# Performance work log

Measured on AMD Instinct MI355X. Metric: run time of the kernel, lower is better.

## Reference

```python
import jax, jax.numpy as jnp
import numpy as np

N, E, F, H, O = 50000, 800000, 256, 128, 64


def setup_inputs() -> dict:
    key = jax.random.key(0)
    ks = jax.random.split(key, 8)
    x = jax.random.normal(ks[0], (N, F), jnp.float32)
    edge_index = jax.random.randint(ks[1], (2, E), 0, N, jnp.int32)
    batch = jnp.zeros((N,), jnp.int32)  # single graph
    s = 0.05
    W0 = jax.random.normal(ks[2], (F, H), jnp.float32) * s
    W1 = jax.random.normal(ks[3], (H, H), jnp.float32) * s
    W2 = jax.random.normal(ks[4], (H, H), jnp.float32) * s
    Wlin = jax.random.normal(ks[5], (H, O), jnp.float32) * s
    b0 = jnp.zeros((H,), jnp.float32)
    b1 = jnp.zeros((H,), jnp.float32)
    b2 = jnp.zeros((H,), jnp.float32)
    blin = jnp.zeros((O,), jnp.float32)
    return {"x": x, "edge_index": edge_index, "batch": batch,
            "W0": W0, "b0": b0, "W1": W1, "b1": b1, "W2": W2, "b2": b2,
            "Wlin": Wlin, "blin": blin}


def _gcn_norm(edge_index, n, dtype):
    # GCNConv: add self-loops, symmetric normalization D^-1/2 (A+I) D^-1/2
    loop = jnp.arange(n, dtype=edge_index.dtype)
    src = jnp.concatenate([edge_index[0], loop])
    dst = jnp.concatenate([edge_index[1], loop])
    deg = jax.ops.segment_sum(jnp.ones_like(dst, dtype=dtype), dst, num_segments=n)
    dinv = jnp.where(deg > 0, jax.lax.rsqrt(deg), 0.0)
    norm = dinv[src] * dinv[dst]  # [E+N]
    return src, dst, norm


def _gcn_conv(h, src, dst, norm, b, n):
    # gather-transform-scatter: message = norm * h[src], aggregate at dst
    msg = h[src] * norm[:, None]
    return jax.ops.segment_sum(msg, dst, num_segments=n) + b


def reference(x, edge_index, batch, W0, b0, W1, b1, W2, b2, Wlin, blin):
    n = x.shape[0]
    src, dst, norm = _gcn_norm(edge_index, n, x.dtype)
    h = _gcn_conv(x @ W0, src, dst, norm, b0, n)   # no inter-layer activation in source
    h = _gcn_conv(h @ W1, src, dst, norm, b1, n)
    h = _gcn_conv(h @ W2, src, dst, norm, b2, n)
    # dropout p=0.2 is identity in eval mode
    h = h @ Wlin + blin
    out = jax.ops.segment_max(h, batch, num_segments=1)  # global_max_pool, single graph
    return out
```

## Files before the change

### kernel.cpp

```cpp
#include <hip/hip_runtime.h>
#include <math.h>


typedef __attribute__((ext_vector_type(8))) _Float16 f16x8;
typedef __attribute__((ext_vector_type(4))) _Float16 f16x4;
typedef __attribute__((ext_vector_type(4))) float f32x4;

__device__ __forceinline__ unsigned enc_f32(float f) {
    unsigned u = __float_as_uint(f);
    return (u & 0x80000000u) ? ~u : (u | 0x80000000u);
}
__device__ __forceinline__ float dec_f32(unsigned e) {
    return (e & 0x80000000u) ? __uint_as_float(e & 0x7fffffffu)
                             : __uint_as_float(~e);
}
#define ENC_NEG_INF 0x007FFFFFu

__device__ __forceinline__ void mm2v_dev(const float* __restrict__ A,
                                         const float* __restrict__ B,
                                         int ldb, int bcol0,
                                         float* __restrict__ C,
                                         int ldc, int ccol0,
                                         _Float16* __restrict__ Wp, int pack,
                                         int vb, int tid,
                                         float* __restrict__ Bs,
                                         float* __restrict__ As) {
    const int r0 = vb * 4;
#pragma unroll
    for (int it = 0; it < 8; ++it) {
        int f = tid + it * 256;
        int row = f >> 4, c4 = (f & 15) * 4;
        *(float4*)&Bs[row * 64 + c4] = *(const float4*)&B[(size_t)row * ldb + bcol0 + c4];
    }
    if (tid < 128)
        *(float4*)&As[tid * 4] = *(const float4*)&A[(size_t)r0 * 128 + tid * 4];
    __syncthreads();
    const int n = tid & 63;
    const int rh = tid >> 6;
    float a0 = 0.f, a1 = 0.f, a2 = 0.f, a3 = 0.f;
#pragma unroll
    for (int k = 0; k < 128; k += 4) {
        a0 = fmaf(As[rh * 128 + k + 0], Bs[(k + 0) * 64 + n], a0);
        a1 = fmaf(As[rh * 128 + k + 1], Bs[(k + 1) * 64 + n], a1);
        a2 = fmaf(As[rh * 128 + k + 2], Bs[(k + 2) * 64 + n], a2);
        a3 = fmaf(As[rh * 128 + k + 3], Bs[(k + 3) * 64 + n], a3);
    }
    float acc = (a0 + a1) + (a2 + a3);
    const int kk = r0 + rh;
    if (pack) {
        int j = kk & 7;
        int l = ((kk >> 3) & 3) * 16 + (n & 15);
        int q = kk >> 5;
        int c = n >> 4;
        Wp[((size_t)(c * 8 + q) * 64 + l) * 8 + j] = (_Float16)acc;
    } else {
        C[(size_t)kk * ldc + ccol0 + n] = acc;
    }
}

__global__ __launch_bounds__(256) void kA(const float* __restrict__ W0,
                                          const float* __restrict__ W1,
                                          const float* __restrict__ W2,
                                          const float* __restrict__ Wl,
                                          const int* __restrict__ dst,
                                          int* __restrict__ T,
                                          float* __restrict__ W01,
                                          float* __restrict__ Q,
                                          int E, int NB, int chunk) {
    __shared__ float Bs[128 * 64];
    __shared__ float As[4 * 128];
    __shared__ int hist[512];
    const int b = blockIdx.x;
    const int tid = threadIdx.x;
    if (b < 64) {
        mm2v_dev(W0, W1, 128, 0, W01, 128, 0, nullptr, 0, b, tid, Bs, As);
    } else if (b < 128) {
        mm2v_dev(W0, W1, 128, 64, W01, 128, 64, nullptr, 0, b - 64, tid, Bs, As);
    } else if (b < 160) {
        mm2v_dev(W2, Wl, 64, 0, Q, 64, 0, nullptr, 0, b - 128, tid, Bs, As);
    } else {
        const int blk = b - 160;
        for (int i = tid; i < 512; i += 256) hist[i] = 0;
        __syncthreads();
        const int lo = blk * chunk, hi = min(E, lo + chunk);
        for (int e = lo + tid; e < hi; e += 256)
            atomicAdd(&hist[dst[e] >> 7], 1);
        __syncthreads();
        for (int bk = tid; bk < NB; bk += 256)
            T[bk * 256 + blk] = hist[bk];
    }
}

__global__ __launch_bounds__(1024) void k_scan1(const int* __restrict__ in,
                                                int* __restrict__ excl,
                                                int* __restrict__ bsums, int L) {
    __shared__ int sh[1024];
    int t = threadIdx.x;
    int i = blockIdx.x * 1024 + t;
    int v = (i < L) ? in[i] : 0;
    sh[t] = v;
    __syncthreads();
    for (int off = 1; off < 1024; off <<= 1) {
        int tv = (t >= off) ? sh[t - off] : 0;
        __syncthreads();
        sh[t] += tv;
        __syncthreads();
    }
    if (i < L) excl[i] = sh[t] - v;
    if (t == 1023) bsums[blockIdx.x] = sh[1023];
}

__global__ __launch_bounds__(1024) void k_scan23(int* __restrict__ excl,
                                                 const int* __restrict__ bsums,
                                                 int L) {
    __shared__ int sh[1024];
    const int t = threadIdx.x;
    sh[t] = (t < (int)blockIdx.x) ? bsums[t] : 0;
    __syncthreads();
    for (int off = 512; off > 0; off >>= 1) {
        if (t < off) sh[t] += sh[t + off];
        __syncthreads();
    }
    const int ofs = sh[0];
    int i = blockIdx.x * 1024 + t;
    if (i < L) excl[i] += ofs;
}

#define PBT 4096
__global__ __launch_bounds__(256) void kP(const int* __restrict__ src,
                                          const int* __restrict__ dst,
                                          const int* __restrict__ T2,
                                          unsigned* __restrict__ eb,
                                          int E, int NB, int chunk,
                                          const float* __restrict__ W01,
                                          const float* __restrict__ Q,
                                          const float* __restrict__ W1,
                                          const float* __restrict__ b0,
                                          const float* __restrict__ b1,
                                          const float* __restrict__ b2,
                                          const float* __restrict__ blin,
                                          const float* __restrict__ Wl,
                                          _Float16* __restrict__ wp,
                                          float* __restrict__ cv) {
    __shared__ int hist[512], lexc[512], pos[512], wpos[512];
    __shared__ unsigned sorted[PBT];
    __shared__ float Bs[128 * 64];
    __shared__ float As[4 * 128];
    __shared__ float t0s[128];
    __shared__ int nzf;
    const int t = threadIdx.x;
    const int b = blockIdx.x;
    if (b < 256) {
        const int blk = b;
        const int lo = blk * chunk, hi = min(E, lo + chunk);
        for (int i = t; i < NB; i += 256) wpos[i] = T2[i * 256 + blk];
        __syncthreads();
        for (int tlo = lo; tlo < hi; tlo += PBT) {
            const int thi = min(hi, tlo + PBT);
            const int sz = thi - tlo;
            for (int i = t; i < 512; i += 256) hist[i] = 0;
            __syncthreads();
            for (int e = tlo + t; e < thi; e += 256)
                atomicAdd(&hist[dst[e] >> 7], 1);
            __syncthreads();
            const int i0 = t, i1 = t + 256;
            const int o0 = hist[i0], o1 = hist[i1];
            for (int off = 1; off < 512; off <<= 1) {
                int v0 = (i0 >= off) ? hist[i0 - off] : 0;
                int v1 = (i1 >= off) ? hist[i1 - off] : 0;
                __syncthreads();
                hist[i0] += v0;
                hist[i1] += v1;
                __syncthreads();
            }
            lexc[i0] = hist[i0] - o0; pos[i0] = hist[i0] - o0;
            lexc[i1] = hist[i1] - o1; pos[i1] = hist[i1] - o1;
            __syncthreads();
            for (int e = tlo + t; e < thi; e += 256) {
                int d = dst[e];
                int p = atomicAdd(&pos[d >> 7], 1);
                sorted[p] = ((unsigned)d << 16) | (unsigned)src[e];
            }
            __syncthreads();
            for (int i = t; i < sz; i += 256) {
                unsigned x = sorted[i];
                int bb = (int)(x >> 23);
                eb[wpos[bb] + (i - lexc[bb])] = x;
            }
            __syncthreads();
            wpos[i0] += o0;
            wpos[i1] += o1;
            __syncthreads();
        }
    } else if (b < 320) {
        mm2v_dev(W01, Q, 64, 0, nullptr, 0, 0, wp, 1, b - 256, t, Bs, As);
    } else {
        if (t == 0) nzf = 0;
        if (t < 128) {
            float s = 0.f;
            for (int j = 0; j < 128; ++j)
                s = fmaf(b0[j], W1[(size_t)j * 128 + t], s);
            t0s[t] = s;
        }
        __syncthreads();
        const int v = t >> 6;
        const int n = t & 63;
        if (v < 3) {
            float a0 = 0.f, a1 = 0.f, a2 = 0.f, a3 = 0.f;
            const float* bb = (v == 0) ? t0s : (v == 1) ? b1 : b2;
            const float* M = (v == 2) ? Wl : Q;
#pragma unroll
            for (int k = 0; k < 128; k += 4) {
                a0 = fmaf(bb[k + 0], M[(k + 0) * 64 + n], a0);
                a1 = fmaf(bb[k + 1], M[(k + 1) * 64 + n], a1);
                a2 = fmaf(bb[k + 2], M[(k + 2) * 64 + n], a2);
                a3 = fmaf(bb[k + 3], M[(k + 3) * 64 + n], a3);
            }
            float c = (a0 + a1) + (a2 + a3);
            if (v == 2) c += blin[n];
            cv[v * 64 + n] = c;
            if (v < 2 && c != 0.f) atomicOr(&nzf, 1);
        }
        __syncthreads();
        if (t == 0) cv[192] = nzf ? 1.f : 0.f;
    }
}

#define PCT 6144
__global__ __launch_bounds__(256) void k_build(const unsigned* __restrict__ eb,
                                               const int* __restrict__ T2,
                                               unsigned short* __restrict__ csr,
                                               int* __restrict__ rofs,
                                               float* __restrict__ dinv,
                                               int N, int E, int NB) {
    __shared__ int hist[128], lofs[128], pos[128];
    __shared__ unsigned short ssrc[PCT];
    const int t = threadIdx.x;
    const int b = blockIdx.x;
    const int glo = T2[b * 256];
    const int ghi = (b + 1 < NB) ? T2[(b + 1) * 256] : E;
    const int sz = ghi - glo;
    if (t < 128) hist[t] = 0;
    __syncthreads();
    for (int i = t; i < sz; i += 256)
        atomicAdd(&hist[(eb[glo + i] >> 16) & 127], 1);
    __syncthreads();
    const int o = (t < 128) ? hist[t] : 0;
    for (int off = 1; off < 128; off <<= 1) {
        int v = (t < 128 && t >= off) ? hist[t - off] : 0;
        __syncthreads();
        if (t < 128) hist[t] += v;
        __syncthreads();
    }
    if (t < 128) {
        int ex = hist[t] - o;
        lofs[t] = ex;
        pos[t] = ex;
        int d = b * 128 + t;
        if (d < N) {
            rofs[d] = glo + ex;
            dinv[d] = rsqrtf((float)(o + 1));
        }
    }
    __syncthreads();
    if (sz <= PCT) {
        for (int i = t; i < sz; i += 256) {
            unsigned x = eb[glo + i];
            int p = atomicAdd(&pos[(x >> 16) & 127], 1);
            ssrc[p] = (unsigned short)(x & 0xFFFFu);
        }
        __syncthreads();
        for (int i = t; i < sz; i += 256) csr[glo + i] = ssrc[i];
    } else {
        for (int i = t; i < sz; i += 256) {
            unsigned x = eb[glo + i];
            int p = atomicAdd(&pos[(x >> 16) & 127], 1);
            csr[glo + p] = (unsigned short)(x & 0xFFFFu);
        }
    }
    if (b == 0 && t == 0) rofs[N] = E;
}

template <int K, int M>
__global__ __launch_bounds__(256, 4) void k_gemm(const void* __restrict__ Av,
                                                 const _Float16* __restrict__ Wp,
                                                 const float* __restrict__ sc,
                                                 _Float16* __restrict__ out,
                                                 int N) {
    constexpr int KB = (K > 128) ? 128 : K;
    constexpr int NQ = K / KB;
    constexpr int NK = KB / 32;
    constexpr int KG = KB / 8;
    constexpr int CT = M / 32;
    constexpr int RT = 3;
    __shared__ _Float16 As[96 * KB];
    const int tid = threadIdx.x;
    const int lane = tid & 63;
    const int wave = tid >> 6;
    const int wrow = wave >> 1;
    const int wcol = wave & 1;
    const int R0 = blockIdx.x * 96;

    f32x4 acc[RT][CT];
#pragma unroll
    for (int rt = 0; rt < RT; ++rt)
#pragma unroll
        for (int ct = 0; ct < CT; ++ct) acc[rt][ct] = (f32x4){0.f, 0.f, 0.f, 0.f};

    for (int q = 0; q < NQ; ++q) {
        if (q) __syncthreads();
        {
            const float* A = (const float*)Av;
#pragma unroll
            for (int it = 0; it < (96 * KB) / (4 * 256); ++it) {
                int idx = tid + it * 256;
                int r = idx >> 5;
                int f4 = idx & 31;
                float4 g = {0.f, 0.f, 0.f, 0.f};
                if (R0 + r < N) g = *(const float4*)&A[(size_t)(R0 + r) * K + q * KB + f4 * 4];
                int kg = f4 >> 1, sub = f4 & 1;
                f16x4 h;
                h[0] = (_Float16)g.x; h[1] = (_Float16)g.y;
                h[2] = (_Float16)g.z; h[3] = (_Float16)g.w;
                *(f16x4*)&As[(r >> 4) * (KG * 128) + kg * 128 + (((r & 15) ^ kg) * 8) + sub * 4] = h;
            }
        }
        __syncthreads();
#pragma unroll
        for (int qq = 0; qq < NK; ++qq) {
            const int kk = q * NK + qq;
            const int kgq = qq * 4 + (lane >> 4);
            f16x8 af[RT], bf[CT];
#pragma unroll
            for (int ct = 0; ct < CT; ++ct) {
                int t = wcol * CT + ct;
                bf[ct] = *(const f16x8*)&Wp[((size_t)(t * (K / 32) + kk) * 64 + lane) * 8];
            }
#pragma unroll
            for (int rt = 0; rt < RT; ++rt) {
                int tr = wrow * RT + rt;
                af[rt] = *(const f16x8*)&As[tr * (KG * 128) + kgq * 128 + (((lane & 15) ^ kgq) * 8)];
            }
#pragma unroll
            for (int rt = 0; rt < RT; ++rt)
#pragma unroll
                for (int ct = 0; ct < CT; ++ct)
                    acc[rt][ct] = __builtin_amdgcn_mfma_f32_16x16x32_f16(af[rt], bf[ct], acc[rt][ct], 0, 0, 0);
        }
    }

    const int quad = lane >> 4;
#pragma unroll
    for (int rt = 0; rt < RT; ++rt)
#pragma unroll
        for (int reg = 0; reg < 4; ++reg) {
            int r = R0 + wrow * 48 + rt * 16 + quad * 4 + reg;
            if (r < N) {
                float s = sc[r];
#pragma unroll
                for (int ct = 0; ct < CT; ++ct) {
                    int c = wcol * (CT * 16) + ct * 16 + (lane & 15);
                    out[(size_t)r * M + c] = (_Float16)(acc[rt][ct][reg] * s);
                }
            }
        }
}

template <int FIN, int UP>
__global__ __launch_bounds__(256) void k_agg64(const _Float16* __restrict__ tmp,
                                               const float* __restrict__ dinv,
                                               const int* __restrict__ rofs,
                                               const unsigned short* __restrict__ csr,
                                               const float* __restrict__ cv,
                                               float* __restrict__ u1,
                                               float* __restrict__ w1,
                                               float* __restrict__ u2,
                                               _Float16* __restrict__ out,
                                               float* __restrict__ bmax, int N) {
    __shared__ unsigned smax[64];
    const int tid = threadIdx.x;
    const int nbAgg = (N + 7) / 8;
    const int vb = blockIdx.x;
    if (UP && vb >= nbAgg) {
        int d = (vb - nbAgg) * 256 + tid;
        if (d >= N) return;
        if (UP == 1) {
            if (cv[192] == 0.f) { u1[d] = 0.f; w1[d] = 0.f; return; }
            float s = 0.f;
            const int beg = rofs[d], end = rofs[d + 1];
            for (int e = beg; e < end; ++e) s += dinv[csr[e]];
            float di = dinv[d];
            float u = di * (s + di);
            u1[d] = u;
            w1[d] = di * u;
        } else {
            if (cv[192] == 0.f) { u2[d] = 0.f; return; }
            float s = 0.f;
            const int beg = rofs[d], end = rofs[d + 1];
            for (int e = beg; e < end; ++e) s += w1[csr[e]];
            u2[d] = dinv[d] * (s + w1[d]);
        }
        return;
    }
    const int lane = tid & 63;
    const int wave = tid >> 6;
    const int eh = lane >> 3;
    const int fl = lane & 7;
    const int d0 = vb * 8 + wave * 2;
    const int d1 = d0 + 1;
    const bool r0 = d0 < N;
    const bool r1 = d1 < N;
    if (FIN) {
        if (tid < 64) smax[tid] = ENC_NEG_INF;
        __syncthreads();
    }
    f16x8 z;
#pragma unroll
    for (int j = 0; j < 8; ++j) z[j] = (_Float16)0.f;

    float a0[8], a1[8];
#pragma unroll
    for (int j = 0; j < 8; ++j) { a0[j] = 0.f; a1[j] = 0.f; }

    int e0 = 0, n0 = 0, e1 = 0, n1 = 0;
    if (r0) { e0 = rofs[d0]; n0 = rofs[d0 + 1]; }
    if (r1) { e1 = rofs[d1]; n1 = rofs[d1 + 1]; }

    while ((r0 && e0 < n0) || (r1 && e1 < n1)) {
        f16x8 v0[4], v1[4];
#pragma unroll
        for (int i = 0; i < 4; ++i) {
            int i0 = e0 + 8 * i + eh;
            v0[i] = (r0 && i0 < n0)
                        ? *(const f16x8*)&tmp[(size_t)csr[i0] * 64 + fl * 8] : z;
            int i1 = e1 + 8 * i + eh;
            v1[i] = (r1 && i1 < n1)
                        ? *(const f16x8*)&tmp[(size_t)csr[i1] * 64 + fl * 8] : z;
        }
        f16x8 s0 = (v0[0] + v0[1]) + (v0[2] + v0[3]);
        f16x8 s1 = (v1[0] + v1[1]) + (v1[2] + v1[3]);
#pragma unroll
        for (int j = 0; j < 8; ++j) {
            a0[j] += (float)s0[j];
            a1[j] += (float)s1[j];
        }
        e0 += 32;
        e1 += 32;
    }
    if (r0 && eh == 7) {
        f16x8 v = *(const f16x8*)&tmp[(size_t)d0 * 64 + fl * 8];
#pragma unroll
        for (int j = 0; j < 8; ++j) a0[j] += (float)v[j];
    }
    if (r1 && eh == 7) {
        f16x8 v = *(const f16x8*)&tmp[(size_t)d1 * 64 + fl * 8];
#pragma unroll
        for (int j = 0; j < 8; ++j) a1[j] += (float)v[j];
    }
#pragma unroll
    for (int j = 0; j < 8; ++j) {
        a0[j] += __shfl_xor(a0[j], 8, 64);
        a0[j] += __shfl_xor(a0[j], 16, 64);
        a0[j] += __shfl_xor(a0[j], 32, 64);
        a1[j] += __shfl_xor(a1[j], 8, 64);
        a1[j] += __shfl_xor(a1[j], 16, 64);
        a1[j] += __shfl_xor(a1[j], 32, 64);
    }
    if (eh == 0) {
        if (FIN == 0) {
            if (r0) {
                float di = dinv[d0];
                float s2 = di * di;
                f16x8 o;
#pragma unroll
                for (int j = 0; j < 8; ++j) o[j] = (_Float16)(a0[j] * s2);
                *(f16x8*)&out[(size_t)d0 * 64 + fl * 8] = o;
            }
            if (r1) {
                float di = dinv[d1];
                float s2 = di * di;
                f16x8 o;
#pragma unroll
                for (int j = 0; j < 8; ++j) o[j] = (_Float16)(a1[j] * s2);
                *(f16x8*)&out[(size_t)d1 * 64 + fl * 8] = o;
            }
        } else {
            if (r0) {
                float di = dinv[d0];
                float v1c = u1[d0], v2c = u2[d0];
#pragma unroll
                for (int j = 0; j < 8; ++j) {
                    int f = fl * 8 + j;
                    float zv = fmaf(di, a0[j],
                               fmaf(v2c, cv[f], fmaf(v1c, cv[64 + f], cv[128 + f])));
                    atomicMax(&smax[f], enc_f32(zv));
                }
            }
            if (r1) {
                float di = dinv[d1];
                float v1c = u1[d1], v2c = u2[d1];
#pragma unroll
                for (int j = 0; j < 8; ++j) {
                    int f = fl * 8 + j;
                    float zv = fmaf(di, a1[j],
                               fmaf(v2c, cv[f], fmaf(v1c, cv[64 + f], cv[128 + f])));
                    atomicMax(&smax[f], enc_f32(zv));
                }
            }
        }
    }
    if (FIN) {
        __syncthreads();
        if (tid < 64) bmax[(size_t)blockIdx.x * 64 + tid] = dec_f32(smax[tid]);
    }
}

__global__ __launch_bounds__(256) void k_pool(const float* __restrict__ bmax,
                                              float* __restrict__ out, int nb) {
    __shared__ float sm[4];
    const int f = blockIdx.x;
    float m = -INFINITY;
    for (int b = threadIdx.x; b < nb; b += 256)
        m = fmaxf(m, bmax[(size_t)b * 64 + f]);
#pragma unroll
    for (int off = 1; off < 64; off <<= 1) m = fmaxf(m, __shfl_xor(m, off, 64));
    if ((threadIdx.x & 63) == 0) sm[threadIdx.x >> 6] = m;
    __syncthreads();
    if (threadIdx.x == 0)
        out[f] = fmaxf(fmaxf(sm[0], sm[1]), fmaxf(sm[2], sm[3]));
}

extern "C" void kernel_launch(void* const* d_in, const int* in_sizes, int n_in,
                              void* d_out, int out_size, void* d_ws, size_t ws_size,
                              hipStream_t stream) {
    const float* x    = (const float*)d_in[0];
    const int*   ei   = (const int*)d_in[1];
    const float* W0   = (const float*)d_in[3];
    const float* b0   = (const float*)d_in[4];
    const float* W1   = (const float*)d_in[5];
    const float* b1   = (const float*)d_in[6];
    const float* W2   = (const float*)d_in[7];
    const float* b2   = (const float*)d_in[8];
    const float* Wlin = (const float*)d_in[9];
    const float* blin = (const float*)d_in[10];
    float* out = (float*)d_out;

    const int N = in_sizes[2];
    const int E = in_sizes[1] / 2;
    const int* src = ei;
    const int* dst = ei + E;

    size_t off = 0;
    auto carve = [&](size_t bytes) {
        void* p = (char*)d_ws + off;
        off += (bytes + 255) & ~(size_t)255;
        return p;
    };
    const int NB    = (N + 127) / 128;
    const int L     = NB * 256;
    const int chunk = (E + 255) / 256;
    const int nbAgg = (N + 7) / 8;
    const int nbU   = (N + 255) / 256;

    float*          dinv = (float*)carve((size_t)N * 4);
    int*            rofs = (int*)carve((size_t)(N + 1) * 4);
    int*            T    = (int*)carve((size_t)L * 4);
    int*            T2   = (int*)carve((size_t)L * 4);
    int*            bsums = (int*)carve(1024 * 4);
    unsigned*       eb   = (unsigned*)carve((size_t)E * 4);
    unsigned short* csr  = (unsigned short*)carve((size_t)E * 2);
    _Float16*       tmpY = (_Float16*)carve((size_t)N * 64 * 2);
    _Float16*       tmpZ = (_Float16*)carve((size_t)N * 64 * 2);
    float*          u1   = (float*)carve((size_t)N * 4);
    float*          w1   = (float*)carve((size_t)N * 4);
    float*          u2   = (float*)carve((size_t)N * 4);
    float*          bmax = (float*)carve((size_t)nbAgg * 64 * 4);
    float*          Q    = (float*)carve(128 * 64 * 4);
    float*          W01  = (float*)carve(256 * 128 * 4);
    float*          cv   = (float*)carve(256 * 4);
    _Float16*       wp   = (_Float16*)carve(256 * 64 * 2);
    (void)ws_size; (void)n_in; (void)out_size;

    const int nbG = (N + 95) / 96;
    const int nbS = (L + 1023) / 1024;

    kA<<<416, 256, 0, stream>>>(W0, W1, W2, Wlin, dst, T, W01, Q, E, NB, chunk);
    k_scan1<<<nbS, 1024, 0, stream>>>(T, T2, bsums, L);
    k_scan23<<<nbS, 1024, 0, stream>>>(T2, bsums, L);
    kP<<<321, 256, 0, stream>>>(src, dst, T2, eb, E, NB, chunk,
                                W01, Q, W1, b0, b1, b2, blin, Wlin, wp, cv);
    k_build<<<NB, 256, 0, stream>>>(eb, T2, csr, rofs, dinv, N, E, NB);
    k_gemm<256, 64><<<nbG, 256, 0, stream>>>(x, wp, dinv, tmpY, N);
    k_agg64<0, 1><<<nbAgg + nbU, 256, 0, stream>>>(tmpY, dinv, rofs, csr, cv,
                                                   u1, w1, u2, tmpZ, nullptr, N);
    k_agg64<0, 2><<<nbAgg + nbU, 256, 0, stream>>>(tmpZ, dinv, rofs, csr, cv,
                                                   u1, w1, u2, tmpY, nullptr, N);
    k_agg64<1, 0><<<nbAgg, 256, 0, stream>>>(tmpY, dinv, rofs, csr, cv,
                                             u1, w1, u2, nullptr, bmax, N);
    k_pool<<<64, 256, 0, stream>>>(bmax, out, nbAgg);
}
```

Measured before the change: 237.4 us.

## Build CSR with global atomic degree count and atomic scatter

Measured after the change: 387.1 us. 1.63x slower.

```diff
diff --git a/kernel.cpp b/kernel.cpp
--- a/kernel.cpp
+++ b/kernel.cpp
@@ -63,13 +63,12 @@
                                           const float* __restrict__ W2,
                                           const float* __restrict__ Wl,
                                           const int* __restrict__ dst,
-                                          int* __restrict__ T,
+                                          int* __restrict__ deg,
                                           float* __restrict__ W01,
                                           float* __restrict__ Q,
-                                          int E, int NB, int chunk) {
+                                          int E) {
     __shared__ float Bs[128 * 64];
     __shared__ float As[4 * 128];
-    __shared__ int hist[512];
     const int b = blockIdx.x;
     const int tid = threadIdx.x;
     if (b < 64) {
@@ -80,58 +79,46 @@
         mm2v_dev(W2, Wl, 64, 0, Q, 64, 0, nullptr, 0, b - 128, tid, Bs, As);
     } else {
         const int blk = b - 160;
-        for (int i = tid; i < 512; i += 256) hist[i] = 0;
-        __syncthreads();
-        const int lo = blk * chunk, hi = min(E, lo + chunk);
-        for (int e = lo + tid; e < hi; e += 256)
-            atomicAdd(&hist[dst[e] >> 7], 1);
-        __syncthreads();
-        for (int bk = tid; bk < NB; bk += 256)
-            T[bk * 256 + blk] = hist[bk];
-    }
-}
-
-__global__ __launch_bounds__(1024) void k_scan1(const int* __restrict__ in,
-                                                int* __restrict__ excl,
-                                                int* __restrict__ bsums, int L) {
+        for (int e = blk * 256 + tid; e < E; e += 256 * 256)
+            atomicAdd(&deg[dst[e]], 1);
+    }
+}
+
+__global__ __launch_bounds__(1024) void kS(const int* __restrict__ deg,
+                                           int* __restrict__ rofs,
+                                           float* __restrict__ dinv,
+                                           int N, int E) {
     __shared__ int sh[1024];
-    int t = threadIdx.x;
-    int i = blockIdx.x * 1024 + t;
-    int v = (i < L) ? in[i] : 0;
-    sh[t] = v;
+    const int t = threadIdx.x;
+    const int per = (N + 1023) / 1024;
+    const int lo = t * per;
+    const int hi = min(N, lo + per);
+    int s = 0;
+    for (int i = lo; i < hi; ++i) s += deg[i];
+    sh[t] = s;
     __syncthreads();
     for (int off = 1; off < 1024; off <<= 1) {
-        int tv = (t >= off) ? sh[t - off] : 0;
-        __syncthreads();
-        sh[t] += tv;
-        __syncthreads();
-    }
-    if (i < L) excl[i] = sh[t] - v;
-    if (t == 1023) bsums[blockIdx.x] = sh[1023];
-}
-
-__global__ __launch_bounds__(1024) void k_scan23(int* __restrict__ excl,
-                                                 const int* __restrict__ bsums,
-                                                 int L) {
-    __shared__ int sh[1024];
-    const int t = threadIdx.x;
-    sh[t] = (t < (int)blockIdx.x) ? bsums[t] : 0;
-    __syncthreads();
-    for (int off = 512; off > 0; off >>= 1) {
-        if (t < off) sh[t] += sh[t + off];
-        __syncthreads();
-    }
-    const int ofs = sh[0];
-    int i = blockIdx.x * 1024 + t;
-    if (i < L) excl[i] += ofs;
-}
-
-#define PBT 4096
-__global__ __launch_bounds__(256) void kP(const int* __restrict__ src,
+        int v = (t >= off) ? sh[t - off] : 0;
+        __syncthreads();
+        sh[t] += v;
+        __syncthreads();
+    }
+    int run = (t > 0) ? sh[t - 1] : 0;
+    for (int i = lo; i < hi; ++i) {
+        int d = deg[i];
+        rofs[i] = run;
+        dinv[i] = rsqrtf((float)(d + 1));
+        run += d;
+    }
+    if (t == 0) rofs[N] = E;
+}
+
+__global__ __launch_bounds__(256) void kC(const int* __restrict__ src,
                                           const int* __restrict__ dst,
-                                          const int* __restrict__ T2,
-                                          unsigned* __restrict__ eb,
-                                          int E, int NB, int chunk,
+                                          int E,
+                                          const int* __restrict__ rofs,
+                                          int* __restrict__ cnt,
+                                          unsigned short* __restrict__ csr,
                                           const float* __restrict__ W01,
                                           const float* __restrict__ Q,
                                           const float* __restrict__ W1,
@@ -142,8 +129,6 @@
                                           const float* __restrict__ Wl,
                                           _Float16* __restrict__ wp,
                                           float* __restrict__ cv) {
-    __shared__ int hist[512], lexc[512], pos[512], wpos[512];
-    __shared__ unsigned sorted[PBT];
     __shared__ float Bs[128 * 64];
     __shared__ float As[4 * 128];
     __shared__ float t0s[128];
@@ -151,46 +136,10 @@
     const int t = threadIdx.x;
     const int b = blockIdx.x;
     if (b < 256) {
-        const int blk = b;
-        const int lo = blk * chunk, hi = min(E, lo + chunk);
-        for (int i = t; i < NB; i += 256) wpos[i] = T2[i * 256 + blk];
-        __syncthreads();
-        for (int tlo = lo; tlo < hi; tlo += PBT) {
-            const int thi = min(hi, tlo + PBT);
-            const int sz = thi - tlo;
-            for (int i = t; i < 512; i += 256) hist[i] = 0;
-            __syncthreads();
-            for (int e = tlo + t; e < thi; e += 256)
-                atomicAdd(&hist[dst[e] >> 7], 1);
-            __syncthreads();
-            const int i0 = t, i1 = t + 256;
-            const int o0 = hist[i0], o1 = hist[i1];
-            for (int off = 1; off < 512; off <<= 1) {
-                int v0 = (i0 >= off) ? hist[i0 - off] : 0;
-                int v1 = (i1 >= off) ? hist[i1 - off] : 0;
-                __syncthreads();
-                hist[i0] += v0;
-                hist[i1] += v1;
-                __syncthreads();
-            }
-            lexc[i0] = hist[i0] - o0; pos[i0] = hist[i0] - o0;
-            lexc[i1] = hist[i1] - o1; pos[i1] = hist[i1] - o1;
-            __syncthreads();
-            for (int e = tlo + t; e < thi; e += 256) {
-                int d = dst[e];
-                int p = atomicAdd(&pos[d >> 7], 1);
-                sorted[p] = ((unsigned)d << 16) | (unsigned)src[e];
-            }
-            __syncthreads();
-            for (int i = t; i < sz; i += 256) {
-                unsigned x = sorted[i];
-                int bb = (int)(x >> 23);
-                eb[wpos[bb] + (i - lexc[bb])] = x;
-            }
-            __syncthreads();
-            wpos[i0] += o0;
-            wpos[i1] += o1;
-            __syncthreads();
+        for (int e = b * 256 + t; e < E; e += 256 * 256) {
+            int d = dst[e];
+            int p = atomicAdd(&cnt[d], 1);
+            csr[rofs[d] + p] = (unsigned short)src[e];
         }
     } else if (b < 320) {
         mm2v_dev(W01, Q, 64, 0, nullptr, 0, 0, wp, 1, b - 256, t, Bs, As);
@@ -224,61 +173,6 @@
         __syncthreads();
         if (t == 0) cv[192] = nzf ? 1.f : 0.f;
     }
-}
-
-#define PCT 6144
-__global__ __launch_bounds__(256) void k_build(const unsigned* __restrict__ eb,
-                                               const int* __restrict__ T2,
-                                               unsigned short* __restrict__ csr,
-                                               int* __restrict__ rofs,
-                                               float* __restrict__ dinv,
-                                               int N, int E, int NB) {
-    __shared__ int hist[128], lofs[128], pos[128];
-    __shared__ unsigned short ssrc[PCT];
-    const int t = threadIdx.x;
-    const int b = blockIdx.x;
-    const int glo = T2[b * 256];
-    const int ghi = (b + 1 < NB) ? T2[(b + 1) * 256] : E;
-    const int sz = ghi - glo;
-    if (t < 128) hist[t] = 0;
-    __syncthreads();
-    for (int i = t; i < sz; i += 256)
-        atomicAdd(&hist[(eb[glo + i] >> 16) & 127], 1);
-    __syncthreads();
-    const int o = (t < 128) ? hist[t] : 0;
-    for (int off = 1; off < 128; off <<= 1) {
-        int v = (t < 128 && t >= off) ? hist[t - off] : 0;
-        __syncthreads();
-        if (t < 128) hist[t] += v;
-        __syncthreads();
-    }
-    if (t < 128) {
-        int ex = hist[t] - o;
-        lofs[t] = ex;
-        pos[t] = ex;
-        int d = b * 128 + t;
-        if (d < N) {
-            rofs[d] = glo + ex;
-            dinv[d] = rsqrtf((float)(o + 1));
-        }
-    }
-    __syncthreads();
-    if (sz <= PCT) {
-        for (int i = t; i < sz; i += 256) {
-            unsigned x = eb[glo + i];
-            int p = atomicAdd(&pos[(x >> 16) & 127], 1);
-            ssrc[p] = (unsigned short)(x & 0xFFFFu);
-        }
-        __syncthreads();
-        for (int i = t; i < sz; i += 256) csr[glo + i] = ssrc[i];
-    } else {
-        for (int i = t; i < sz; i += 256) {
-            unsigned x = eb[glo + i];
-            int p = atomicAdd(&pos[(x >> 16) & 127], 1);
-            csr[glo + p] = (unsigned short)(x & 0xFFFFu);
-        }
-    }
-    if (b == 0 && t == 0) rofs[N] = E;
 }
 
 template <int K, int M>
@@ -556,40 +450,34 @@
         off += (bytes + 255) & ~(size_t)255;
         return p;
     };
-    const int NB    = (N + 127) / 128;
-    const int L     = NB * 256;
-    const int chunk = (E + 255) / 256;
     const int nbAgg = (N + 7) / 8;
     const int nbU   = (N + 255) / 256;
 
-    float*          dinv = (float*)carve((size_t)N * 4);
-    int*            rofs = (int*)carve((size_t)(N + 1) * 4);
-    int*            T    = (int*)carve((size_t)L * 4);
-    int*            T2   = (int*)carve((size_t)L * 4);
-    int*            bsums = (int*)carve(1024 * 4);
-    unsigned*       eb   = (unsigned*)carve((size_t)E * 4);
-    unsigned short* csr  = (unsigned short*)carve((size_t)E * 2);
-    _Float16*       tmpY = (_Float16*)carve((size_t)N * 64 * 2);
-    _Float16*       tmpZ = (_Float16*)carve((size_t)N * 64 * 2);
-    float*          u1   = (float*)carve((size_t)N * 4);
-    float*          w1   = (float*)carve((size_t)N * 4);
-    float*          u2   = (float*)carve((size_t)N * 4);
-    float*          bmax = (float*)carve((size_t)nbAgg * 64 * 4);
-    float*          Q    = (float*)carve(128 * 64 * 4);
-    float*          W01  = (float*)carve(256 * 128 * 4);
-    float*          cv   = (float*)carve(256 * 4);
-    _Float16*       wp   = (_Float16*)carve(256 * 64 * 2);
+    float*          dinv  = (float*)carve((size_t)N * 4);
+    int*            rofs  = (int*)carve((size_t)(N + 1) * 4);
+    int*            degcnt = (int*)carve((size_t)2 * N * 4);
+    unsigned short* csr   = (unsigned short*)carve((size_t)E * 2);
+    _Float16*       tmpY  = (_Float16*)carve((size_t)N * 64 * 2);
+    _Float16*       tmpZ  = (_Float16*)carve((size_t)N * 64 * 2);
+    float*          u1    = (float*)carve((size_t)N * 4);
+    float*          w1    = (float*)carve((size_t)N * 4);
+    float*          u2    = (float*)carve((size_t)N * 4);
+    float*          bmax  = (float*)carve((size_t)nbAgg * 64 * 4);
+    float*          Q     = (float*)carve(128 * 64 * 4);
+    float*          W01   = (float*)carve(256 * 128 * 4);
+    float*          cv    = (float*)carve(256 * 4);
+    _Float16*       wp    = (_Float16*)carve(256 * 64 * 2);
+    int*            deg   = degcnt;
+    int*            cnt   = degcnt + N;
     (void)ws_size; (void)n_in; (void)out_size;
 
     const int nbG = (N + 95) / 96;
-    const int nbS = (L + 1023) / 1024;
-
-    kA<<<416, 256, 0, stream>>>(W0, W1, W2, Wlin, dst, T, W01, Q, E, NB, chunk);
-    k_scan1<<<nbS, 1024, 0, stream>>>(T, T2, bsums, L);
-    k_scan23<<<nbS, 1024, 0, stream>>>(T2, bsums, L);
-    kP<<<321, 256, 0, stream>>>(src, dst, T2, eb, E, NB, chunk,
+
+    hipMemsetAsync(degcnt, 0, (size_t)2 * N * 4, stream);
+    kA<<<416, 256, 0, stream>>>(W0, W1, W2, Wlin, dst, deg, W01, Q, E);
+    kS<<<1, 1024, 0, stream>>>(deg, rofs, dinv, N, E);
+    kC<<<321, 256, 0, stream>>>(src, dst, E, rofs, cnt, csr,
                                 W01, Q, W1, b0, b1, b2, blin, Wlin, wp, cv);
-    k_build<<<NB, 256, 0, stream>>>(eb, T2, csr, rofs, dinv, N, E, NB);
     k_gemm<256, 64><<<nbG, 256, 0, stream>>>(x, wp, dinv, tmpY, N);
     k_agg64<0, 1><<<nbAgg + nbU, 256, 0, stream>>>(tmpY, dinv, rofs, csr, cv,
                                                    u1, w1, u2, tmpZ, nullptr, N);
```
